# Performance work log

Hardware: AMD Instinct MI355X
Metric: run time of the kernel (lower is better)

The kernel has to match this reference:

```python
import jax, jax.numpy as jnp
import numpy as np

HEADS = 4
DIM_HEAD = 32
SCALE = DIM_HEAD ** -0.5


def setup_inputs() -> dict:
    key = jax.random.key(0)
    k1, k2, k3 = jax.random.split(key, 3)
    dim = 128
    hidden = HEADS * DIM_HEAD  # 128
    x = jax.random.normal(k1, (4, dim, 64, 64), dtype=jnp.float32)
    w_qkv = jax.random.normal(k2, (3 * hidden, dim), dtype=jnp.float32) * (dim ** -0.5)
    w_out = jax.random.normal(k3, (dim, hidden), dtype=jnp.float32) * (hidden ** -0.5)
    b_out = jnp.zeros((dim,), dtype=jnp.float32)
    return {"x": x, "w_qkv": w_qkv, "w_out": w_out, "b_out": b_out}


def reference(x, w_qkv, w_out, b_out):
    b, c, h, w = x.shape
    n = h * w
    # 1x1 conv == channel matmul per pixel
    qkv = jnp.einsum('oc,bchw->bohw', w_qkv, x)  # [b, 3*hidden, h, w]
    q, k, v = jnp.split(qkv, 3, axis=1)
    # b (heads d) x y -> b heads d (x y)
    def to_heads(t):
        return t.reshape(b, HEADS, DIM_HEAD, n)
    q = to_heads(q) * SCALE
    k = to_heads(k)
    v = to_heads(v)
    sim = jnp.einsum('bhdi,bhdj->bhij', q, k)          # [b, heads, n, n]
    attn = jax.nn.softmax(sim, axis=-1)
    out = jnp.einsum('bhij,bhdj->bhid', attn, v)        # [b, heads, n, d]
    # b h (x y) d -> b (h d) x y
    out = out.transpose(0, 1, 3, 2).reshape(b, HEADS * DIM_HEAD, h, w)
    out = jnp.einsum('oc,bchw->bohw', w_out, out) + b_out[None, :, None, None]
    return out
```

## Files before the change

### kernel.cpp

```cpp
#include <hip/hip_runtime.h>
#include <math.h>

#define NHEAD 4
#define DHEAD 32
#define NPIX  4096
#define CIN   128

typedef __bf16 bf16_t;
typedef __bf16 bf16x8 __attribute__((ext_vector_type(8)));
typedef __bf16 bf16x4 __attribute__((ext_vector_type(4)));
typedef float  f32x4  __attribute__((ext_vector_type(4)));

constexpr float QSCALE = 0.17677669529663687f * 1.4426950408889634f;

__global__ void __launch_bounds__(256) prep_swz(
    const float* __restrict__ wqkv, const float* __restrict__ wout,
    ushort* __restrict__ wq_s, ushort* __restrict__ wo_s) {
  const int gid = blockIdx.x * 256 + threadIdx.x;
  const int lane = gid & 63, n = lane & 15, quad = (lane >> 4) & 3;
  if (gid < 6144) {
    const int ot = gid >> 8, k = (gid >> 6) & 3;
    const float sc = (ot < 8) ? QSCALE : 1.f;
    const float* src = wqkv + (size_t)(ot * 16 + n) * CIN + k * 32 + quad * 8;
    bf16x8 o;
#pragma unroll
    for (int e = 0; e < 8; ++e) o[e] = (bf16_t)(src[e] * sc);
    *(bf16x8*)(wq_s + (size_t)gid * 8) = o;
  } else {
    const int oid = gid - 6144;
    const int ot = oid >> 8, k = (oid >> 6) & 3;
    const float* src = wout + (size_t)(ot * 16 + n) * CIN + k * 32 + quad * 8;
    bf16x8 o;
#pragma unroll
    for (int e = 0; e < 8; ++e) o[e] = (bf16_t)src[e];
    *(bf16x8*)(wo_s + (size_t)oid * 8) = o;
  }
}

__global__ void __launch_bounds__(256) qkv_mfma(
    const float* __restrict__ x, const ushort* __restrict__ wq_s,
    ushort* __restrict__ qb, ushort* __restrict__ kb, ushort* __restrict__ vT) {
  __shared__ ushort Xls[32 * 136];
  const int blk = blockIdx.x, tid = threadIdx.x;
  const int wave = tid >> 6, lane = tid & 63;
  const int n = lane & 15, quad = lane >> 4;
  const int bb = blk >> 7;
  const int p0 = (blk & 127) * 32;

  {
    const int pc = tid & 7, c0 = (tid >> 3) * 4;
    const float* xp = x + ((size_t)bb * CIN + c0) * NPIX + p0 + pc * 4;
    float4 r0 = *(const float4*)xp;
    float4 r1 = *(const float4*)(xp + NPIX);
    float4 r2 = *(const float4*)(xp + 2 * NPIX);
    float4 r3 = *(const float4*)(xp + 3 * NPIX);
    bf16x4 w0 = {(bf16_t)r0.x, (bf16_t)r1.x, (bf16_t)r2.x, (bf16_t)r3.x};
    bf16x4 w1 = {(bf16_t)r0.y, (bf16_t)r1.y, (bf16_t)r2.y, (bf16_t)r3.y};
    bf16x4 w2 = {(bf16_t)r0.z, (bf16_t)r1.z, (bf16_t)r2.z, (bf16_t)r3.z};
    bf16x4 w3 = {(bf16_t)r0.w, (bf16_t)r1.w, (bf16_t)r2.w, (bf16_t)r3.w};
    *(bf16x4*)&Xls[(pc * 4 + 0) * 136 + c0] = w0;
    *(bf16x4*)&Xls[(pc * 4 + 1) * 136 + c0] = w1;
    *(bf16x4*)&Xls[(pc * 4 + 2) * 136 + c0] = w2;
    *(bf16x4*)&Xls[(pc * 4 + 3) * 136 + c0] = w3;
  }
  __syncthreads();

  bf16x8 xf[2][4];
#pragma unroll
  for (int nt = 0; nt < 2; ++nt)
#pragma unroll
    for (int k = 0; k < 4; ++k)
      xf[nt][k] = *(const bf16x8*)&Xls[(nt * 16 + n) * 136 + k * 32 + quad * 8];

#pragma unroll
  for (int mt = 0; mt < 6; ++mt) {
    const int ot = wave * 6 + mt;
    const int type = ot >> 3;
    const int wt = ot & 7, head = wt >> 1, d0 = (wt & 1) * 16;
    const int bh = bb * NHEAD + head;
    bf16x8 wf4[4];
#pragma unroll
    for (int k = 0; k < 4; ++k)
      wf4[k] = *(const bf16x8*)(wq_s + (size_t)((ot * 4 + k) * 64 + lane) * 8);
    f32x4 acc[2] = {{0.f, 0.f, 0.f, 0.f}, {0.f, 0.f, 0.f, 0.f}};
    if (type < 2) {
#pragma unroll
      for (int k = 0; k < 4; ++k)
#pragma unroll
        for (int nt = 0; nt < 2; ++nt)
          acc[nt] = __builtin_amdgcn_mfma_f32_16x16x32_bf16(wf4[k], xf[nt][k], acc[nt], 0, 0, 0);
      ushort* dst = (type == 0) ? qb : kb;
#pragma unroll
      for (int nt = 0; nt < 2; ++nt) {
        bf16x4 o = {(bf16_t)acc[nt][0], (bf16_t)acc[nt][1],
                    (bf16_t)acc[nt][2], (bf16_t)acc[nt][3]};
        *(bf16x4*)(dst + ((size_t)bh * NPIX + p0 + nt * 16 + n) * DHEAD + d0 + quad * 4) = o;
      }
    } else {
#pragma unroll
      for (int k = 0; k < 4; ++k)
#pragma unroll
        for (int nt = 0; nt < 2; ++nt)
          acc[nt] = __builtin_amdgcn_mfma_f32_16x16x32_bf16(xf[nt][k], wf4[k], acc[nt], 0, 0, 0);
#pragma unroll
      for (int nt = 0; nt < 2; ++nt) {
        bf16x4 o = {(bf16_t)acc[nt][0], (bf16_t)acc[nt][1],
                    (bf16_t)acc[nt][2], (bf16_t)acc[nt][3]};
        *(bf16x4*)(vT + ((size_t)bh * DHEAD + d0 + n) * NPIX + p0 + nt * 16 + quad * 4) = o;
      }
    }
  }
}

__device__ __forceinline__ void ft_load(const ushort* kb0, const ushort* vb0,
                                        int t, bf16x8* kf, bf16x8* vf) {
#pragma unroll
  for (int p = 0; p < 2; ++p) {
#pragma unroll
    for (int s = 0; s < 2; ++s)
      kf[p * 2 + s] = *(const bf16x8*)(kb0 + (size_t)(t * 64 + p * 32 + s * 4) * DHEAD);
#pragma unroll
    for (int dp = 0; dp < 2; ++dp)
      vf[p * 2 + dp] = *(const bf16x8*)(vb0 + (size_t)dp * 16 * NPIX + t * 64 + p * 32);
  }
}

__device__ __forceinline__ void ft_compute(const bf16x8* qf, const bf16x8* kf,
                                           const bf16x8* vf, const bf16x8 ones,
                                           f32x4 O[8][2], f32x4* Ol) {
  const f32x4 zero = {0.f, 0.f, 0.f, 0.f};
#pragma unroll
  for (int p = 0; p < 2; ++p) {
#pragma unroll
    for (int rp = 0; rp < 8; ++rp) {
      f32x4 sa = __builtin_amdgcn_mfma_f32_16x16x32_bf16(kf[p * 2 + 0], qf[rp], zero, 0, 0, 0);
      f32x4 sb = __builtin_amdgcn_mfma_f32_16x16x32_bf16(kf[p * 2 + 1], qf[rp], zero, 0, 0, 0);
      bf16x8 pf;
#pragma unroll
      for (int r = 0; r < 4; ++r) {
        pf[r]     = (bf16_t)__builtin_amdgcn_exp2f(sa[r]);
        pf[r + 4] = (bf16_t)__builtin_amdgcn_exp2f(sb[r]);
      }
      O[rp][0] = __builtin_amdgcn_mfma_f32_16x16x32_bf16(pf, vf[p * 2 + 0], O[rp][0], 0, 0, 0);
      O[rp][1] = __builtin_amdgcn_mfma_f32_16x16x32_bf16(pf, vf[p * 2 + 1], O[rp][1], 0, 0, 0);
      Ol[rp]   = __builtin_amdgcn_mfma_f32_16x16x32_bf16(pf, ones, Ol[rp], 0, 0, 0);
    }
  }
}

__global__ void __launch_bounds__(256, 2) flash_mfma(
    const ushort* __restrict__ qb, const ushort* __restrict__ kbuf,
    const ushort* __restrict__ vTb, float* __restrict__ part) {
  const int tid = threadIdx.x, wave = tid >> 6, lane = tid & 63;
  const int n = lane & 15, quad = lane >> 4;

  const int id = blockIdx.x;
  const int g  = (id & 7) | ((id >> 6) << 3);
  const int qbk = (id >> 3) & 7;
  const int bh = g >> 2;
  const int js = g & 3;
  const int qrel = qbk * 512 + wave * 128;

  const ushort* kg = kbuf + (size_t)bh * NPIX * DHEAD;
  const ushort* vg = vTb + (size_t)bh * DHEAD * NPIX;

  bf16x8 qf[8];
#pragma unroll
  for (int rp = 0; rp < 8; ++rp)
    qf[rp] = *(const bf16x8*)(qb +
        ((size_t)bh * NPIX + qrel + rp * 16 + n) * DHEAD + quad * 8);

  f32x4 O[8][2], Ol[8];
#pragma unroll
  for (int rp = 0; rp < 8; ++rp) {
    O[rp][0] = (f32x4){0.f, 0.f, 0.f, 0.f};
    O[rp][1] = (f32x4){0.f, 0.f, 0.f, 0.f};
    Ol[rp]   = (f32x4){0.f, 0.f, 0.f, 0.f};
  }
  const bf16_t one = (bf16_t)1.0f;
  const bf16x8 ones = {one, one, one, one, one, one, one, one};

  const int pk = ((n >> 2) << 3) | (n & 3);
  const ushort* kb0 = kg + (size_t)(js * 1024 + pk) * DHEAD + quad * 8;
  const ushort* vb0 = vg + (size_t)n * NPIX + js * 1024 + quad * 8;

  bf16x8 kA[4], vA[4], kB[4], vB[4];
  ft_load(kb0, vb0, 0, kA, vA);
#pragma unroll 1
  for (int t = 0; t < 16; t += 2) {
    ft_load(kb0, vb0, t + 1, kB, vB);
    ft_compute(qf, kA, vA, ones, O, Ol);
    if (t + 2 < 16) ft_load(kb0, vb0, t + 2, kA, vA);
    ft_compute(qf, kB, vB, ones, O, Ol);
  }

  float* pb = part + ((size_t)js * 65536 + (size_t)bh * NPIX + qrel) * 36;
#pragma unroll
  for (int rp = 0; rp < 8; ++rp)
#pragma unroll
    for (int r = 0; r < 4; ++r) {
      const int q = rp * 16 + quad * 4 + r;
      pb[(size_t)q * 36 + n]      = O[rp][0][r];
      pb[(size_t)q * 36 + 16 + n] = O[rp][1][r];
      if (n == 0) pb[(size_t)q * 36 + 32] = Ol[rp][r];
    }
}

__global__ void __launch_bounds__(256) out_fused(
    const float* __restrict__ part, const ushort* __restrict__ wo_s,
    const float* __restrict__ bias, float* __restrict__ out) {
  __shared__ ushort AOls[32 * 136];
  const int blk = blockIdx.x, tid = threadIdx.x;
  const int wave = tid >> 6, lane = tid & 63;
  const int n = lane & 15, quad = lane >> 4;
  const int bb = blk >> 7;
  const int p0 = (blk & 127) * 32;
  const int oc0 = wave * 32;

  bf16x8 wf[2][4];
#pragma unroll
  for (int mt = 0; mt < 2; ++mt)
#pragma unroll
    for (int k = 0; k < 4; ++k)
      wf[mt][k] = *(const bf16x8*)(wo_s + (size_t)(((wave * 2 + mt) * 4 + k) * 64 + lane) * 8);

  {
    const int px8 = tid >> 3, c8 = tid & 7;
    const int h = c8 >> 1, dh = (c8 & 1) * 16;
    const size_t rowbase = (size_t)(bb * NHEAD + h) * NPIX + p0 + px8;
    float s[16];
#pragma unroll
    for (int e = 0; e < 16; ++e) s[e] = 0.f;
    float l = 0.f;
#pragma unroll
    for (int js = 0; js < 4; ++js) {
      const float* pp = part + ((size_t)js * 65536 + rowbase) * 36;
      f32x4 a0 = *(const f32x4*)(pp + dh);
      f32x4 a1 = *(const f32x4*)(pp + dh + 4);
      f32x4 a2 = *(const f32x4*)(pp + dh + 8);
      f32x4 a3 = *(const f32x4*)(pp + dh + 12);
#pragma unroll
      for (int e = 0; e < 4; ++e) {
        s[e]      += a0[e];
        s[4 + e]  += a1[e];
        s[8 + e]  += a2[e];
        s[12 + e] += a3[e];
      }
      l += pp[32];
    }
    const float inv = 1.f / l;
    bf16x8 o0, o1;
#pragma unroll
    for (int e = 0; e < 8; ++e) {
      o0[e] = (bf16_t)(s[e] * inv);
      o1[e] = (bf16_t)(s[8 + e] * inv);
    }
    ushort* dstl = &AOls[px8 * 136 + (c8 >> 1) * 32 + (c8 & 1) * 16];
    *(bf16x8*)dstl = o0;
    *(bf16x8*)(dstl + 8) = o1;
  }
  __syncthreads();

  bf16x8 bfr[2][4];
#pragma unroll
  for (int nt = 0; nt < 2; ++nt)
#pragma unroll
    for (int k = 0; k < 4; ++k)
      bfr[nt][k] = *(const bf16x8*)&AOls[(nt * 16 + n) * 136 + k * 32 + quad * 8];

  f32x4 acc[2][2];
#pragma unroll
  for (int mt = 0; mt < 2; ++mt)
#pragma unroll
    for (int nt = 0; nt < 2; ++nt) acc[mt][nt] = (f32x4){0.f, 0.f, 0.f, 0.f};
#pragma unroll
  for (int k = 0; k < 4; ++k)
#pragma unroll
    for (int mt = 0; mt < 2; ++mt)
#pragma unroll
      for (int nt = 0; nt < 2; ++nt)
        acc[mt][nt] = __builtin_amdgcn_mfma_f32_16x16x32_bf16(
            wf[mt][k], bfr[nt][k], acc[mt][nt], 0, 0, 0);

#pragma unroll
  for (int mt = 0; mt < 2; ++mt) {
    const int oc = oc0 + mt * 16 + quad * 4;
#pragma unroll
    for (int nt = 0; nt < 2; ++nt)
#pragma unroll
      for (int r = 0; r < 4; ++r)
        out[((size_t)bb * CIN + oc + r) * NPIX + p0 + nt * 16 + n] =
            acc[mt][nt][r] + bias[oc + r];
  }
}

extern "C" void kernel_launch(void* const* d_in, const int* in_sizes, int n_in,
                              void* d_out, int out_size, void* d_ws, size_t ws_size,
                              hipStream_t stream) {
  const float* x     = (const float*)d_in[0];
  const float* w_qkv = (const float*)d_in[1];
  const float* w_out = (const float*)d_in[2];
  const float* b_out = (const float*)d_in[3];
  float* out = (float*)d_out;

  char* base = (char*)d_ws;
  ushort* qb   = (ushort*)base;
  ushort* kb   = (ushort*)(base + (size_t)4 * 1024 * 1024);
  ushort* vT   = (ushort*)(base + (size_t)8 * 1024 * 1024);
  ushort* wq_s = (ushort*)(base + (size_t)12 * 1024 * 1024);
  ushort* wo_s = (ushort*)(base + (size_t)12 * 1024 * 1024 + 256 * 1024);
  float*  part = (float*)(base + (size_t)13 * 1024 * 1024);

  prep_swz<<<dim3(32), 256, 0, stream>>>(w_qkv, w_out, wq_s, wo_s);
  qkv_mfma<<<dim3(512), 256, 0, stream>>>(x, wq_s, qb, kb, vT);
  flash_mfma<<<dim3(512), 256, 0, stream>>>(qb, kb, vT, part);
  out_fused<<<dim3(512), 256, 0, stream>>>(part, wo_s, b_out, out);
}
```

Baseline: 128.3 us.

## Split QKV and output projection kernels across more blocks; raise MFMA priority

The QKV projection kernel now launches a 2-D grid, so each block computes half of the output tiles. This doubles block count but reloads and converts the x tile twice. The output projection kernel now processes 16 pixels per block instead of 32, doubling the grid to spread the partial-reduction loads across more CUs. The flash attention inner compute loop is wrapped in s_setprio to favour MFMA issue over other waves' memory work.

```diff
diff --git a/kernel.cpp b/kernel.cpp
--- a/kernel.cpp
+++ b/kernel.cpp
@@ -42,6 +42,7 @@
     ushort* __restrict__ qb, ushort* __restrict__ kb, ushort* __restrict__ vT) {
   __shared__ ushort Xls[32 * 136];
   const int blk = blockIdx.x, tid = threadIdx.x;
+  const int half = blockIdx.y;
   const int wave = tid >> 6, lane = tid & 63;
   const int n = lane & 15, quad = lane >> 4;
   const int bb = blk >> 7;
@@ -73,8 +74,8 @@
       xf[nt][k] = *(const bf16x8*)&Xls[(nt * 16 + n) * 136 + k * 32 + quad * 8];
 
 #pragma unroll
-  for (int mt = 0; mt < 6; ++mt) {
-    const int ot = wave * 6 + mt;
+  for (int mt = 0; mt < 3; ++mt) {
+    const int ot = half * 12 + wave * 3 + mt;
     const int type = ot >> 3;
     const int wt = ot & 7, head = wt >> 1, d0 = (wt & 1) * 16;
     const int bh = bb * NHEAD + head;
@@ -129,6 +130,7 @@
                                            const bf16x8* vf, const bf16x8 ones,
                                            f32x4 O[8][2], f32x4* Ol) {
   const f32x4 zero = {0.f, 0.f, 0.f, 0.f};
+  __builtin_amdgcn_s_setprio(1);
 #pragma unroll
   for (int p = 0; p < 2; ++p) {
 #pragma unroll
@@ -146,6 +148,7 @@
       Ol[rp]   = __builtin_amdgcn_mfma_f32_16x16x32_bf16(pf, ones, Ol[rp], 0, 0, 0);
     }
   }
+  __builtin_amdgcn_s_setprio(0);
 }
 
 __global__ void __launch_bounds__(256, 2) flash_mfma(
@@ -209,12 +212,12 @@
 __global__ void __launch_bounds__(256) out_fused(
     const float* __restrict__ part, const ushort* __restrict__ wo_s,
     const float* __restrict__ bias, float* __restrict__ out) {
-  __shared__ ushort AOls[32 * 136];
+  __shared__ ushort AOls[16 * 136];
   const int blk = blockIdx.x, tid = threadIdx.x;
   const int wave = tid >> 6, lane = tid & 63;
   const int n = lane & 15, quad = lane >> 4;
-  const int bb = blk >> 7;
-  const int p0 = (blk & 127) * 32;
+  const int bb = blk >> 8;
+  const int p0 = (blk & 255) * 16;
   const int oc0 = wave * 32;
 
   bf16x8 wf[2][4];
@@ -225,72 +228,55 @@
       wf[mt][k] = *(const bf16x8*)(wo_s + (size_t)(((wave * 2 + mt) * 4 + k) * 64 + lane) * 8);
 
   {
-    const int px8 = tid >> 3, c8 = tid & 7;
-    const int h = c8 >> 1, dh = (c8 & 1) * 16;
-    const size_t rowbase = (size_t)(bb * NHEAD + h) * NPIX + p0 + px8;
-    float s[16];
-#pragma unroll
-    for (int e = 0; e < 16; ++e) s[e] = 0.f;
+    const int px = tid >> 4, c16 = tid & 15;
+    const int h = c16 >> 2, doff = (c16 & 3) * 8;
+    const size_t rowbase = (size_t)(bb * NHEAD + h) * NPIX + p0 + px;
+    float s[8];
+#pragma unroll
+    for (int e = 0; e < 8; ++e) s[e] = 0.f;
     float l = 0.f;
 #pragma unroll
     for (int js = 0; js < 4; ++js) {
       const float* pp = part + ((size_t)js * 65536 + rowbase) * 36;
-      f32x4 a0 = *(const f32x4*)(pp + dh);
-      f32x4 a1 = *(const f32x4*)(pp + dh + 4);
-      f32x4 a2 = *(const f32x4*)(pp + dh + 8);
-      f32x4 a3 = *(const f32x4*)(pp + dh + 12);
+      f32x4 a0 = *(const f32x4*)(pp + doff);
+      f32x4 a1 = *(const f32x4*)(pp + doff + 4);
 #pragma unroll
       for (int e = 0; e < 4; ++e) {
-        s[e]      += a0[e];
-        s[4 + e]  += a1[e];
-        s[8 + e]  += a2[e];
-        s[12 + e] += a3[e];
+        s[e]     += a0[e];
+        s[4 + e] += a1[e];
       }
       l += pp[32];
     }
     const float inv = 1.f / l;
-    bf16x8 o0, o1;
-#pragma unroll
-    for (int e = 0; e < 8; ++e) {
-      o0[e] = (bf16_t)(s[e] * inv);
-      o1[e] = (bf16_t)(s[8 + e] * inv);
-    }
-    ushort* dstl = &AOls[px8 * 136 + (c8 >> 1) * 32 + (c8 & 1) * 16];
-    *(bf16x8*)dstl = o0;
-    *(bf16x8*)(dstl + 8) = o1;
+    bf16x8 o0;
+#pragma unroll
+    for (int e = 0; e < 8; ++e) o0[e] = (bf16_t)(s[e] * inv);
+    *(bf16x8*)&AOls[px * 136 + c16 * 8] = o0;
   }
   __syncthreads();
 
-  bf16x8 bfr[2][4];
-#pragma unroll
-  for (int nt = 0; nt < 2; ++nt)
-#pragma unroll
-    for (int k = 0; k < 4; ++k)
-      bfr[nt][k] = *(const bf16x8*)&AOls[(nt * 16 + n) * 136 + k * 32 + quad * 8];
-
-  f32x4 acc[2][2];
-#pragma unroll
-  for (int mt = 0; mt < 2; ++mt)
-#pragma unroll
-    for (int nt = 0; nt < 2; ++nt) acc[mt][nt] = (f32x4){0.f, 0.f, 0.f, 0.f};
+  bf16x8 bfr[4];
 #pragma unroll
   for (int k = 0; k < 4; ++k)
+    bfr[k] = *(const bf16x8*)&AOls[n * 136 + k * 32 + quad * 8];
+
+  f32x4 acc[2];
+#pragma unroll
+  for (int mt = 0; mt < 2; ++mt) acc[mt] = (f32x4){0.f, 0.f, 0.f, 0.f};
+#pragma unroll
+  for (int k = 0; k < 4; ++k)
 #pragma unroll
     for (int mt = 0; mt < 2; ++mt)
-#pragma unroll
-      for (int nt = 0; nt < 2; ++nt)
-        acc[mt][nt] = __builtin_amdgcn_mfma_f32_16x16x32_bf16(
-            wf[mt][k], bfr[nt][k], acc[mt][nt], 0, 0, 0);
+      acc[mt] = __builtin_amdgcn_mfma_f32_16x16x32_bf16(
+          wf[mt][k], bfr[k], acc[mt], 0, 0, 0);
 
 #pragma unroll
   for (int mt = 0; mt < 2; ++mt) {
     const int oc = oc0 + mt * 16 + quad * 4;
 #pragma unroll
-    for (int nt = 0; nt < 2; ++nt)
-#pragma unroll
-      for (int r = 0; r < 4; ++r)
-        out[((size_t)bb * CIN + oc + r) * NPIX + p0 + nt * 16 + n] =
-            acc[mt][nt][r] + bias[oc + r];
+    for (int r = 0; r < 4; ++r)
+      out[((size_t)bb * CIN + oc + r) * NPIX + p0 + n] =
+          acc[mt][r] + bias[oc + r];
   }
 }
 
@@ -312,7 +298,7 @@
   float*  part = (float*)(base + (size_t)13 * 1024 * 1024);
 
   prep_swz<<<dim3(32), 256, 0, stream>>>(w_qkv, w_out, wq_s, wo_s);
-  qkv_mfma<<<dim3(512), 256, 0, stream>>>(x, wq_s, qb, kb, vT);
+  qkv_mfma<<<dim3(512, 2), 256, 0, stream>>>(x, wq_s, qb, kb, vT);
   flash_mfma<<<dim3(512), 256, 0, stream>>>(qb, kb, vT, part);
-  out_fused<<<dim3(512), 256, 0, stream>>>(part, wo_s, b_out, out);
-}
+  out_fused<<<dim3(1024), 256, 0, stream>>>(part, wo_s, b_out, out);
+}
```

New measurement: 125.6 us. 1.02x faster.
